# Kernel optimization log

Hardware: AMD Instinct MI355X
Metric: run time of the kernel (lower is better)

Reference implementation:

```python
import jax, jax.numpy as jnp
import numpy as np

B, S, D, H, O, E = 2, 2048, 1024, 2048, 1024, 8


def setup_inputs() -> dict:
    key = jax.random.key(0)
    k_x, k_rw, k_w1, k_w3, k_w2 = jax.random.split(key, 5)
    sD = 1.0 / np.sqrt(D)
    sH = 1.0 / np.sqrt(H)
    return {
        "x": jax.random.normal(k_x, (B, S, D), dtype=jnp.float32),
        "router_w": jax.random.normal(k_rw, (E, D), dtype=jnp.float32) * sD,  # nn.Linear(D, E).weight
        "router_b": jnp.zeros((E,), dtype=jnp.float32),
        "W1": jax.random.normal(k_w1, (E, D, H), dtype=jnp.float32) * sD,  # per-expert w1 (x @ W1)
        "W3": jax.random.normal(k_w3, (E, D, H), dtype=jnp.float32) * sD,  # per-expert gate w3
        "W2": jax.random.normal(k_w2, (E, H, O), dtype=jnp.float32) * sH,  # per-expert down-proj
        "top_k": 2,
    }


def reference(x, router_w, router_b, W1, W3, W2, top_k):
    b, s, d = x.shape
    xf = x.reshape(-1, d)  # [T, D], T = B*S
    T = xf.shape[0]

    # Router: softmax over experts, then top-k and renormalize
    logits = xf @ router_w.T + router_b            # [T, E]
    probs = jax.nn.softmax(logits, axis=-1)
    top_p, top_i = jax.lax.top_k(probs, top_k)     # [T, k]
    top_p = top_p / top_p.sum(axis=-1, keepdims=True)

    # Dense all-expert SwiGLU MLPs (faithful to reference: every expert on every token)
    h = jnp.einsum('td,edh->eth', xf, W1)          # [E, T, H]
    g = jnp.einsum('td,edh->eth', xf, W3)          # [E, T, H]
    eo = jnp.einsum('eth,eho->eto', jax.nn.silu(h) * g, W2)  # [E, T, O]

    # Gather each token's top-k expert outputs and combine
    sel = eo[top_i, jnp.arange(T)[:, None]]        # [T, k, O]
    out = jnp.sum(top_p[..., None] * sel, axis=1)  # [T, O]
    return out.reshape(b, s, -1)
```

## Files before the change

kernel.cpp:

```cpp
#include <hip/hip_runtime.h>
#include <hip/hip_bf16.h>

#define TTOK 4096
#define DIM  1024
#define HID  2048
#define ODIM 1024
#define NE   8

typedef __attribute__((ext_vector_type(8))) short  short8;
typedef __attribute__((ext_vector_type(4))) float  f32x4;
typedef __attribute__((ext_vector_type(8))) unsigned short ushort8;

#define WAITVM(N) asm volatile("s_waitcnt vmcnt(" #N ")" ::: "memory")
#define BAR() __builtin_amdgcn_s_barrier()

__device__ __forceinline__ unsigned short f2bf(float f){
  unsigned u = __float_as_uint(f);
  u += 0x7fffu + ((u >> 16) & 1u);
  return (unsigned short)(u >> 16);
}

__device__ __forceinline__ void gld16(const void* g, void* l){
  __builtin_amdgcn_global_load_lds(
      (const __attribute__((address_space(1))) unsigned int*)g,
      (__attribute__((address_space(3))) unsigned int*)l, 16, 0, 0);
}

__global__ __launch_bounds__(256) void router_kernel(
    const float* __restrict__ x, const float* __restrict__ rw,
    const float* __restrict__ rb, unsigned short* __restrict__ xbf,
    int2* __restrict__ toke, float2* __restrict__ tokw)
{
  int tok  = (blockIdx.x * blockDim.x + threadIdx.x) >> 6;
  int lane = threadIdx.x & 63;
  const float4* xr = (const float4*)(x + (size_t)tok * DIM + lane * 16);
  float xv[16];
#pragma unroll
  for (int q = 0; q < 4; q++){
    float4 v = xr[q];
    xv[q*4+0]=v.x; xv[q*4+1]=v.y; xv[q*4+2]=v.z; xv[q*4+3]=v.w;
  }
  ushort8 u0, u1;
#pragma unroll
  for (int j = 0; j < 8; j++){ u0[j] = f2bf(xv[j]); u1[j] = f2bf(xv[8+j]); }
  ushort8* xo = (ushort8*)(xbf + (size_t)tok * DIM + lane * 16);
  xo[0] = u0; xo[1] = u1;

  float lg[NE];
#pragma unroll
  for (int e = 0; e < NE; e++){
    const float4* wr4 = (const float4*)(rw + (size_t)e * DIM + lane * 16);
    float s = 0.f;
#pragma unroll
    for (int q = 0; q < 4; q++){
      float4 wv = wr4[q];
      s += xv[q*4+0]*wv.x + xv[q*4+1]*wv.y + xv[q*4+2]*wv.z + xv[q*4+3]*wv.w;
    }
    lg[e] = s;
  }
#pragma unroll
  for (int e = 0; e < NE; e++)
    for (int s = 1; s < 64; s <<= 1) lg[e] += __shfl_xor(lg[e], s, 64);

  if (lane == 0){
#pragma unroll
    for (int e = 0; e < NE; e++) lg[e] += rb[e];
    int e0 = 0; float l0 = lg[0];
    for (int e = 1; e < NE; e++) if (lg[e] > l0){ l0 = lg[e]; e0 = e; }
    int e1 = -1; float l1 = -1e30f;
    for (int e = 0; e < NE; e++) if (e != e0 && lg[e] > l1){ l1 = lg[e]; e1 = e; }
    float w0 = 1.f / (1.f + __expf(l1 - l0));
    float w1 = 1.f / (1.f + __expf(l0 - l1));
    toke[tok] = make_int2(e0, e1);
    tokw[tok] = make_float2(w0, w1);
  }
}

__global__ __launch_bounds__(256) void plan_kernel(
    const int2* __restrict__ toke, const float2* __restrict__ tokw,
    int* __restrict__ counts, int* __restrict__ offs,
    int* __restrict__ tlist, float* __restrict__ wlist)
{
  const int e  = blockIdx.x;
  const int t  = threadIdx.x;
  const int lane = t & 63, wv = t >> 6;
  __shared__ int sh[4 * 8];
  __shared__ int tot[8];
  __shared__ int sw[4];

  int wcnt[NE];
#pragma unroll
  for (int ee = 0; ee < NE; ee++) wcnt[ee] = 0;
  for (int base = 0; base < TTOK; base += 256){
    int2 p = toke[base + t];
#pragma unroll
    for (int ee = 0; ee < NE; ee++){
      unsigned long long m = __ballot(p.x == ee || p.y == ee);
      if (lane == 0) wcnt[ee] += __popcll(m);
    }
  }
  if (lane == 0){
#pragma unroll
    for (int ee = 0; ee < NE; ee++) sh[wv * 8 + ee] = wcnt[ee];
  }
  __syncthreads();
  if (t < NE) tot[t] = sh[t] + sh[8 + t] + sh[16 + t] + sh[24 + t];
  __syncthreads();

  int my_off = 0;
#pragma unroll
  for (int ee = 0; ee < NE; ee++) if (ee < e) my_off += tot[ee];

  if (e == 0 && t < NE){
    counts[t] = tot[t];
    int o = 0;
    for (int ee = 0; ee < NE; ee++){ if (ee < t) o += tot[ee]; }
    offs[t] = o;
    if (t == 0){
      int s = 0;
      for (int ee = 0; ee < NE; ee++) s += tot[ee];
      offs[NE] = s;
    }
  }

  int running = my_off;
  for (int base = 0; base < TTOK; base += 256){
    int tokid = base + t;
    int2  p = toke[tokid];
    float2 wgt = tokw[tokid];
    bool s0 = (p.x == e), s1 = (p.y == e);
    bool flag = s0 || s1;
    unsigned long long m = __ballot(flag);
    int rank_in_wave = __popcll(m & ((lane == 0) ? 0ull : ((~0ull) >> (64 - lane))));
    if (lane == 0) sw[wv] = __popcll(m);
    __syncthreads();
    int wave_base = 0, tot4 = 0;
#pragma unroll
    for (int w2 = 0; w2 < 4; w2++){ int v = sw[w2]; tot4 += v; if (w2 < wv) wave_base += v; }
    if (flag){
      int pos = running + wave_base + rank_in_wave;
      tlist[pos] = tokid;
      wlist[pos] = s0 ? wgt.x : wgt.y;
    }
    running += tot4;
    __syncthreads();
  }
}

__global__ __launch_bounds__(256) void transpose_cvt(
    const float* __restrict__ in, unsigned short* __restrict__ out, int R, int C)
{
  __shared__ __align__(16) unsigned short tl[64 * 128];
  int e = blockIdx.z;
  const float* src = in + (size_t)e * R * C + (size_t)(blockIdx.y * 128) * C + blockIdx.x * 64;
  unsigned short* dst = out + (size_t)e * C * R + (size_t)(blockIdx.x * 64) * R + blockIdx.y * 128;
  int t = threadIdx.x;
#pragma unroll
  for (int i = 0; i < 8; i++){
    int idx = i * 256 + t;
    int c = idx & 63, r0 = (idx >> 6) * 4;
    unsigned short v[4];
#pragma unroll
    for (int j = 0; j < 4; j++) v[j] = f2bf(src[(size_t)(r0 + j) * C + c]);
    unsigned long long pk = (unsigned long long)v[0] | ((unsigned long long)v[1] << 16)
      | ((unsigned long long)v[2] << 32) | ((unsigned long long)v[3] << 48);
    *(unsigned long long*)((char*)tl + c * 256 + (((r0 >> 3) ^ (c & 15)) * 16) + (r0 & 7) * 2) = pk;
  }
  __syncthreads();
#pragma unroll
  for (int i = 0; i < 4; i++){
    int idx = i * 256 + t;
    int c = idx >> 4, r0 = (idx & 15) * 8;
    ushort8 u = *(const ushort8*)((const char*)tl + c * 256 + (((r0 >> 3) ^ (c & 15)) * 16));
    *(ushort8*)(dst + (size_t)c * R + r0) = u;
  }
}

__global__ __launch_bounds__(256,2) void ffn1_kernel(
    const unsigned short* __restrict__ xbf,
    const unsigned short* __restrict__ w1t,
    const unsigned short* __restrict__ w3t,
    unsigned short* __restrict__ abuf,
    const int* __restrict__ counts, const int* __restrict__ offs,
    const int* __restrict__ tlist)
{
  const int e = blockIdx.x, ct = blockIdx.y, rt = blockIdx.z;
  const int cnt = counts[e];
  const int rbase = rt * 128;
  if (rbase >= cnt) return;
  const int off = offs[e];
  const int rows_left = cnt - rbase;
  const int t = threadIdx.x;
  const int lane = t & 63, w = t >> 6;
  const int wr = w >> 1, wc = w & 1;

  __shared__ __align__(16) unsigned short lds[3 * 12288];

  int ar0 = t >> 2, ar1 = 64 + (t >> 2);
  int psw = (t & 3) ^ ((t >> 3) & 3);
  int ra0 = ar0 < rows_left ? ar0 : rows_left - 1;
  int ra1 = ar1 < rows_left ? ar1 : rows_left - 1;
  int tok0 = tlist[off + rbase + ra0];
  int tok1 = tlist[off + rbase + ra1];
  const char* sA0  = (const char*)xbf + ((size_t)tok0 * DIM) * 2 + psw * 16;
  const char* sA1  = (const char*)xbf + ((size_t)tok1 * DIM) * 2 + psw * 16;
  const char* sB10 = (const char*)w1t + (((size_t)e * HID + ct * 128 + ar0) * DIM) * 2 + psw * 16;
  const char* sB11 = (const char*)w1t + (((size_t)e * HID + ct * 128 + ar1) * DIM) * 2 + psw * 16;
  const char* sB30 = (const char*)w3t + (((size_t)e * HID + ct * 128 + ar0) * DIM) * 2 + psw * 16;
  const char* sB31 = (const char*)w3t + (((size_t)e * HID + ct * 128 + ar1) * DIM) * 2 + psw * 16;
  const int dofs = w * 1024;

  auto STAGE = [&](int bs, int kt){
    int kb = kt << 6;
    char* base = (char*)lds + bs * 24576;
    gld16(sA0  + kb, base +            dofs);
    gld16(sA1  + kb, base +  4096 +    dofs);
    gld16(sB10 + kb, base +  8192 +    dofs);
    gld16(sB11 + kb, base + 12288 +    dofs);
    gld16(sB30 + kb, base + 16384 +    dofs);
    gld16(sB31 + kb, base + 20480 +    dofs);
  };

  const int chsw = ((lane >> 4) ^ ((lane >> 1) & 3)) * 8;
  int aofs[4], b1ofs[4], b3ofs[4];
#pragma unroll
  for (int i = 0; i < 4; i++){
    int am = wr * 64 + i * 16 + (lane & 15);
    int bn = wc * 64 + i * 16 + (lane & 15);
    aofs[i]  = am * 32 + chsw;
    b1ofs[i] = 4096 + bn * 32 + chsw;
    b3ofs[i] = 8192 + bn * 32 + chsw;
  }

  f32x4 acch[4][4], accg[4][4];
#pragma unroll
  for (int i = 0; i < 4; i++)
#pragma unroll
    for (int j = 0; j < 4; j++){
      acch[i][j] = (f32x4){0.f,0.f,0.f,0.f};
      accg[i][j] = (f32x4){0.f,0.f,0.f,0.f};
    }

  auto COMPUTE = [&](int bs){
    const unsigned short* L = lds + bs * 12288;
    short8 a[4], b1[4], b3[4];
#pragma unroll
    for (int i = 0; i < 4; i++){
      a[i]  = *(const short8*)(L + aofs[i]);
      b1[i] = *(const short8*)(L + b1ofs[i]);
      b3[i] = *(const short8*)(L + b3ofs[i]);
    }
    __builtin_amdgcn_s_setprio(1);
#pragma unroll
    for (int mi = 0; mi < 4; mi++)
#pragma unroll
      for (int ni = 0; ni < 4; ni++){
        acch[mi][ni] = __builtin_amdgcn_mfma_f32_16x16x32_bf16(a[mi], b1[ni], acch[mi][ni], 0, 0, 0);
        accg[mi][ni] = __builtin_amdgcn_mfma_f32_16x16x32_bf16(a[mi], b3[ni], accg[mi][ni], 0, 0, 0);
      }
    __builtin_amdgcn_s_setprio(0);
  };

  STAGE(0, 0); STAGE(1, 1); STAGE(2, 2);
  int cur = 0;
  for (int kt = 0; kt < DIM / 32 - 3; ++kt){
    WAITVM(12); BAR();
    COMPUTE(cur);
    BAR();
    STAGE(cur, kt + 3);
    cur = (cur == 2) ? 0 : cur + 1;
  }
  WAITVM(12); BAR(); COMPUTE(cur); BAR(); cur = (cur == 2) ? 0 : cur + 1;
  WAITVM(6);  BAR(); COMPUTE(cur); BAR(); cur = (cur == 2) ? 0 : cur + 1;
  WAITVM(0);  BAR(); COMPUTE(cur);

#pragma unroll
  for (int mi = 0; mi < 4; mi++)
#pragma unroll
    for (int r = 0; r < 4; r++){
      int row_local = wr * 64 + mi * 16 + ((lane >> 4) << 2) + r;
      if (row_local < rows_left){
        size_t pair = (size_t)(off + rbase + row_local);
        unsigned short* arow = abuf + pair * HID + ct * 128 + wc * 64 + (lane & 15);
#pragma unroll
        for (int ni = 0; ni < 4; ni++){
          float h = acch[mi][ni][r], g = accg[mi][ni][r];
          float sv = h / (1.f + __expf(-h));
          arow[ni * 16] = f2bf(sv * g);
        }
      }
    }
}

__global__ __launch_bounds__(256,3) void ffn2_kernel(
    const unsigned short* __restrict__ abuf,
    const unsigned short* __restrict__ w2t,
    float* __restrict__ dout,
    const int* __restrict__ counts, const int* __restrict__ offs,
    const int* __restrict__ tlist, const float* __restrict__ wlist)
{
  const int e = blockIdx.x, ct = blockIdx.y, rt = blockIdx.z;
  const int cnt = counts[e];
  const int rbase = rt * 128;
  if (rbase >= cnt) return;
  const int off = offs[e];
  const int rows_left = cnt - rbase;
  const int t = threadIdx.x;
  const int lane = t & 63, w = t >> 6;
  const int wr = w >> 1, wc = w & 1;

  __shared__ __align__(16) unsigned short lds[3 * 8192];

  int ar0 = t >> 2, ar1 = 64 + (t >> 2);
  int psw = (t & 3) ^ ((t >> 3) & 3);
  int ra0 = ar0 < rows_left ? ar0 : rows_left - 1;
  int ra1 = ar1 < rows_left ? ar1 : rows_left - 1;
  const char* sA0 = (const char*)abuf + ((size_t)(off + rbase + ra0) * HID) * 2 + psw * 16;
  const char* sA1 = (const char*)abuf + ((size_t)(off + rbase + ra1) * HID) * 2 + psw * 16;
  const char* sB0 = (const char*)w2t + (((size_t)e * ODIM + ct * 128 + ar0) * HID) * 2 + psw * 16;
  const char* sB1 = (const char*)w2t + (((size_t)e * ODIM + ct * 128 + ar1) * HID) * 2 + psw * 16;
  const int dofs = w * 1024;

  auto STAGE = [&](int bs, int kt){
    int kb = kt << 6;
    char* base = (char*)lds + bs * 16384;
    gld16(sA0 + kb, base +           dofs);
    gld16(sA1 + kb, base +  4096 +   dofs);
    gld16(sB0 + kb, base +  8192 +   dofs);
    gld16(sB1 + kb, base + 12288 +   dofs);
  };

  const int chsw = ((lane >> 4) ^ ((lane >> 1) & 3)) * 8;
  int aofs[4], bofs[4];
#pragma unroll
  for (int i = 0; i < 4; i++){
    int am = wr * 64 + i * 16 + (lane & 15);
    int bn = wc * 64 + i * 16 + (lane & 15);
    aofs[i] = am * 32 + chsw;
    bofs[i] = 4096 + bn * 32 + chsw;
  }

  f32x4 acc[4][4];
#pragma unroll
  for (int i = 0; i < 4; i++)
#pragma unroll
    for (int j = 0; j < 4; j++) acc[i][j] = (f32x4){0.f,0.f,0.f,0.f};

  auto COMPUTE = [&](int bs){
    const unsigned short* L = lds + bs * 8192;
    short8 a[4], b[4];
#pragma unroll
    for (int i = 0; i < 4; i++){
      a[i] = *(const short8*)(L + aofs[i]);
      b[i] = *(const short8*)(L + bofs[i]);
    }
    __builtin_amdgcn_s_setprio(1);
#pragma unroll
    for (int mi = 0; mi < 4; mi++)
#pragma unroll
      for (int ni = 0; ni < 4; ni++)
        acc[mi][ni] = __builtin_amdgcn_mfma_f32_16x16x32_bf16(a[mi], b[ni], acc[mi][ni], 0, 0, 0);
    __builtin_amdgcn_s_setprio(0);
  };

  STAGE(0, 0); STAGE(1, 1); STAGE(2, 2);
  int cur = 0;
  for (int kt = 0; kt < HID / 32 - 3; ++kt){
    WAITVM(8); BAR();
    COMPUTE(cur);
    BAR();
    STAGE(cur, kt + 3);
    cur = (cur == 2) ? 0 : cur + 1;
  }
  WAITVM(8); BAR(); COMPUTE(cur); BAR(); cur = (cur == 2) ? 0 : cur + 1;
  WAITVM(4); BAR(); COMPUTE(cur); BAR(); cur = (cur == 2) ? 0 : cur + 1;
  WAITVM(0); BAR(); COMPUTE(cur);

#pragma unroll
  for (int mi = 0; mi < 4; mi++)
#pragma unroll
    for (int r = 0; r < 4; r++){
      int row_local = wr * 64 + mi * 16 + ((lane >> 4) << 2) + r;
      if (row_local < rows_left){
        int pair = off + rbase + row_local;
        int token = tlist[pair];
        float p   = wlist[pair];
        float* orow = dout + (size_t)token * ODIM + ct * 128 + wc * 64 + (lane & 15);
#pragma unroll
        for (int ni = 0; ni < 4; ni++)
          atomicAdd(orow + ni * 16, p * acc[mi][ni][r]);
      }
    }
}

extern "C" void kernel_launch(void* const* d_in, const int* in_sizes, int n_in,
                              void* d_out, int out_size, void* d_ws, size_t ws_size,
                              hipStream_t stream)
{
  const float* x  = (const float*)d_in[0];
  const float* rw = (const float*)d_in[1];
  const float* rb = (const float*)d_in[2];
  const float* W1 = (const float*)d_in[3];
  const float* W3 = (const float*)d_in[4];
  const float* W2 = (const float*)d_in[5];

  char* ws = (char*)d_ws;
  const size_t off_ctrl = 0;
  const size_t off_toke = 256;
  const size_t off_tokw = off_toke + (size_t)TTOK * 8;
  const size_t off_tl   = off_tokw + (size_t)TTOK * 8;
  const size_t off_wl   = off_tl   + (size_t)2 * TTOK * 4;
  const size_t off_xbf  = off_wl   + (size_t)2 * TTOK * 4;
  const size_t off_w1t  = off_xbf  + (size_t)TTOK * DIM * 2;
  const size_t off_w3t  = off_w1t  + (size_t)NE * HID * DIM * 2;
  const size_t off_w2t  = off_w3t  + (size_t)NE * HID * DIM * 2;
  const size_t off_ab   = off_w2t  + (size_t)NE * ODIM * HID * 2;
  const size_t need     = off_ab   + (size_t)2 * TTOK * HID * 2;
  if (ws_size < need) return;

  int* counts = (int*)(ws + off_ctrl);
  int* offs   = (int*)(ws + off_ctrl + 64);
  int2*   toke = (int2*)  (ws + off_toke);
  float2* tokw = (float2*)(ws + off_tokw);
  int*    tl   = (int*)   (ws + off_tl);
  float*  wl   = (float*) (ws + off_wl);
  unsigned short* xbf = (unsigned short*)(ws + off_xbf);
  unsigned short* w1t = (unsigned short*)(ws + off_w1t);
  unsigned short* w3t = (unsigned short*)(ws + off_w3t);
  unsigned short* w2t = (unsigned short*)(ws + off_w2t);
  unsigned short* ab  = (unsigned short*)(ws + off_ab);

  hipMemsetAsync(d_out, 0, (size_t)out_size * sizeof(float), stream);

  router_kernel<<<TTOK / 4, 256, 0, stream>>>(x, rw, rb, xbf, toke, tokw);
  plan_kernel<<<NE, 256, 0, stream>>>(toke, tokw, counts, offs, tl, wl);

  transpose_cvt<<<dim3(HID / 64, DIM / 128, NE), 256, 0, stream>>>(W1, w1t, DIM, HID);
  transpose_cvt<<<dim3(HID / 64, DIM / 128, NE), 256, 0, stream>>>(W3, w3t, DIM, HID);
  transpose_cvt<<<dim3(ODIM / 64, HID / 128, NE), 256, 0, stream>>>(W2, w2t, HID, ODIM);

  ffn1_kernel<<<dim3(NE, HID / 128, 32), 256, 0, stream>>>(xbf, w1t, w3t, ab, counts, offs, tl);
  ffn2_kernel<<<dim3(NE, ODIM / 128, 32), 256, 0, stream>>>(ab, w2t, (float*)d_out, counts, offs, tl, wl);
}
```

Measured before the change: 253.8 us.

## Switch FFN GEMMs to double buffering, raise occupancy, and swizzle block order

Both expert GEMM kernels drop from triple-buffered to double-buffered LDS and issue the next stage's loads before computing the current one. The smaller LDS footprint lets launch bounds rise from 2 to 3 blocks per CU for ffn1 and from 3 to 4 for ffn2. The 3D grid becomes a 1D grid with an explicit mapping that interleaves experts across consecutive blocks and groups column/row tiles for better L2 reuse. The cost is a shallower prefetch depth and tighter register budgets, which could cause spills or expose more memory latency.

Result: slower. 449.3 us (+77.0%).

```diff
diff --git a/kernel.cpp b/kernel.cpp
--- a/kernel.cpp
+++ b/kernel.cpp
@@ -176,7 +176,7 @@
   }
 }
 
-__global__ __launch_bounds__(256,2) void ffn1_kernel(
+__global__ __launch_bounds__(256,3) void ffn1_kernel(
     const unsigned short* __restrict__ xbf,
     const unsigned short* __restrict__ w1t,
     const unsigned short* __restrict__ w3t,
@@ -184,7 +184,12 @@
     const int* __restrict__ counts, const int* __restrict__ offs,
     const int* __restrict__ tlist)
 {
-  const int e = blockIdx.x, ct = blockIdx.y, rt = blockIdx.z;
+  const int wgid = blockIdx.x;
+  const int e = wgid & 7;
+  const int j = wgid >> 3;
+  const int u = j & 15, g = j >> 4;
+  const int ct = (g & 7) * 2 + (u >> 3);
+  const int rt = (g >> 3) * 8 + (u & 7);
   const int cnt = counts[e];
   const int rbase = rt * 128;
   if (rbase >= cnt) return;
@@ -194,7 +199,7 @@
   const int lane = t & 63, w = t >> 6;
   const int wr = w >> 1, wc = w & 1;
 
-  __shared__ __align__(16) unsigned short lds[3 * 12288];
+  __shared__ __align__(16) unsigned short lds[2 * 12288];
 
   int ar0 = t >> 2, ar1 = 64 + (t >> 2);
   int psw = (t & 3) ^ ((t >> 3) & 3);
@@ -236,9 +241,9 @@
 #pragma unroll
   for (int i = 0; i < 4; i++)
 #pragma unroll
-    for (int j = 0; j < 4; j++){
-      acch[i][j] = (f32x4){0.f,0.f,0.f,0.f};
-      accg[i][j] = (f32x4){0.f,0.f,0.f,0.f};
+    for (int jj = 0; jj < 4; jj++){
+      acch[i][jj] = (f32x4){0.f,0.f,0.f,0.f};
+      accg[i][jj] = (f32x4){0.f,0.f,0.f,0.f};
     }
 
   auto COMPUTE = [&](int bs){
@@ -261,18 +266,16 @@
     __builtin_amdgcn_s_setprio(0);
   };
 
-  STAGE(0, 0); STAGE(1, 1); STAGE(2, 2);
-  int cur = 0;
-  for (int kt = 0; kt < DIM / 32 - 3; ++kt){
-    WAITVM(12); BAR();
-    COMPUTE(cur);
+  STAGE(0, 0);
+  int kt = 0;
+  for (; kt < DIM / 32 - 1; ++kt){
+    STAGE((kt + 1) & 1, kt + 1);
+    WAITVM(6); BAR();
+    COMPUTE(kt & 1);
     BAR();
-    STAGE(cur, kt + 3);
-    cur = (cur == 2) ? 0 : cur + 1;
-  }
-  WAITVM(12); BAR(); COMPUTE(cur); BAR(); cur = (cur == 2) ? 0 : cur + 1;
-  WAITVM(6);  BAR(); COMPUTE(cur); BAR(); cur = (cur == 2) ? 0 : cur + 1;
-  WAITVM(0);  BAR(); COMPUTE(cur);
+  }
+  WAITVM(0); BAR();
+  COMPUTE(kt & 1);
 
 #pragma unroll
   for (int mi = 0; mi < 4; mi++)
@@ -284,22 +287,27 @@
         unsigned short* arow = abuf + pair * HID + ct * 128 + wc * 64 + (lane & 15);
 #pragma unroll
         for (int ni = 0; ni < 4; ni++){
-          float h = acch[mi][ni][r], g = accg[mi][ni][r];
+          float h = acch[mi][ni][r], gg = accg[mi][ni][r];
           float sv = h / (1.f + __expf(-h));
-          arow[ni * 16] = f2bf(sv * g);
+          arow[ni * 16] = f2bf(sv * gg);
         }
       }
     }
 }
 
-__global__ __launch_bounds__(256,3) void ffn2_kernel(
+__global__ __launch_bounds__(256,4) void ffn2_kernel(
     const unsigned short* __restrict__ abuf,
     const unsigned short* __restrict__ w2t,
     float* __restrict__ dout,
     const int* __restrict__ counts, const int* __restrict__ offs,
     const int* __restrict__ tlist, const float* __restrict__ wlist)
 {
-  const int e = blockIdx.x, ct = blockIdx.y, rt = blockIdx.z;
+  const int wgid = blockIdx.x;
+  const int e = wgid & 7;
+  const int j = wgid >> 3;
+  const int u = j & 7, g = j >> 3;
+  const int ct = (g & 3) * 2 + (u >> 2);
+  const int rt = (g >> 2) * 4 + (u & 3);
   const int cnt = counts[e];
   const int rbase = rt * 128;
   if (rbase >= cnt) return;
@@ -309,7 +317,7 @@
   const int lane = t & 63, w = t >> 6;
   const int wr = w >> 1, wc = w & 1;
 
-  __shared__ __align__(16) unsigned short lds[3 * 8192];
+  __shared__ __align__(16) unsigned short lds[2 * 8192];
 
   int ar0 = t >> 2, ar1 = 64 + (t >> 2);
   int psw = (t & 3) ^ ((t >> 3) & 3);
@@ -344,7 +352,7 @@
 #pragma unroll
   for (int i = 0; i < 4; i++)
 #pragma unroll
-    for (int j = 0; j < 4; j++) acc[i][j] = (f32x4){0.f,0.f,0.f,0.f};
+    for (int jj = 0; jj < 4; jj++) acc[i][jj] = (f32x4){0.f,0.f,0.f,0.f};
 
   auto COMPUTE = [&](int bs){
     const unsigned short* L = lds + bs * 8192;
@@ -363,18 +371,16 @@
     __builtin_amdgcn_s_setprio(0);
   };
 
-  STAGE(0, 0); STAGE(1, 1); STAGE(2, 2);
-  int cur = 0;
-  for (int kt = 0; kt < HID / 32 - 3; ++kt){
-    WAITVM(8); BAR();
-    COMPUTE(cur);
+  STAGE(0, 0);
+  int kt = 0;
+  for (; kt < HID / 32 - 1; ++kt){
+    STAGE((kt + 1) & 1, kt + 1);
+    WAITVM(4); BAR();
+    COMPUTE(kt & 1);
     BAR();
-    STAGE(cur, kt + 3);
-    cur = (cur == 2) ? 0 : cur + 1;
-  }
-  WAITVM(8); BAR(); COMPUTE(cur); BAR(); cur = (cur == 2) ? 0 : cur + 1;
-  WAITVM(4); BAR(); COMPUTE(cur); BAR(); cur = (cur == 2) ? 0 : cur + 1;
-  WAITVM(0); BAR(); COMPUTE(cur);
+  }
+  WAITVM(0); BAR();
+  COMPUTE(kt & 1);
 
 #pragma unroll
   for (int mi = 0; mi < 4; mi++)
@@ -439,6 +445,6 @@
   transpose_cvt<<<dim3(HID / 64, DIM / 128, NE), 256, 0, stream>>>(W3, w3t, DIM, HID);
   transpose_cvt<<<dim3(ODIM / 64, HID / 128, NE), 256, 0, stream>>>(W2, w2t, HID, ODIM);
 
-  ffn1_kernel<<<dim3(NE, HID / 128, 32), 256, 0, stream>>>(xbf, w1t, w3t, ab, counts, offs, tl);
-  ffn2_kernel<<<dim3(NE, ODIM / 128, 32), 256, 0, stream>>>(ab, w2t, (float*)d_out, counts, offs, tl, wl);
-}
+  ffn1_kernel<<<NE * 16 * 32, 256, 0, stream>>>(xbf, w1t, w3t, ab, counts, offs, tl);
+  ffn2_kernel<<<NE * 8 * 32, 256, 0, stream>>>(ab, w2t, (float*)d_out, counts, offs, tl, wl);
+}
```

## Pre-gather routed tokens contiguously and remap FFN block order for L2 locality

Applied to the files above, without the earlier changes.

Adds a gather kernel that copies each routed token's bf16 activation row into a contiguous per-expert buffer, so the first FFN kernel streams A tiles linearly instead of following token indices. Both FFN kernels switch to a 1D grid with a swizzled mapping that keeps blocks of the same expert and nearby row/column tiles adjacent in launch order, aimed at better L2 reuse of weights and activations. The cost is an extra launch plus a write and read of a gathered activation buffer.

Result: slower. 272.9 us (+7.6%).

```diff
diff --git a/kernel.cpp b/kernel.cpp
--- a/kernel.cpp
+++ b/kernel.cpp
@@ -147,6 +147,18 @@
   }
 }
 
+__global__ __launch_bounds__(256) void gather_kernel(
+    const unsigned short* __restrict__ xbf, const int* __restrict__ tlist,
+    unsigned short* __restrict__ xg)
+{
+  int pair = blockIdx.x * 4 + (threadIdx.x >> 6);
+  int lane = threadIdx.x & 63;
+  int tok  = tlist[pair];
+  const ushort8* s = (const ushort8*)(xbf + (size_t)tok * DIM + lane * 16);
+  ushort8* d = (ushort8*)(xg + (size_t)pair * DIM + lane * 16);
+  d[0] = s[0]; d[1] = s[1];
+}
+
 __global__ __launch_bounds__(256) void transpose_cvt(
     const float* __restrict__ in, unsigned short* __restrict__ out, int R, int C)
 {
@@ -177,14 +189,18 @@
 }
 
 __global__ __launch_bounds__(256,2) void ffn1_kernel(
-    const unsigned short* __restrict__ xbf,
+    const unsigned short* __restrict__ xg,
     const unsigned short* __restrict__ w1t,
     const unsigned short* __restrict__ w3t,
     unsigned short* __restrict__ abuf,
-    const int* __restrict__ counts, const int* __restrict__ offs,
-    const int* __restrict__ tlist)
-{
-  const int e = blockIdx.x, ct = blockIdx.y, rt = blockIdx.z;
+    const int* __restrict__ counts, const int* __restrict__ offs)
+{
+  const int wgid = blockIdx.x;
+  const int e = wgid & 7;
+  const int j = wgid >> 3;
+  const int u = j & 15, g = j >> 4;
+  const int ct = (g & 7) * 2 + (u >> 3);
+  const int rt = (g >> 3) * 8 + (u & 7);
   const int cnt = counts[e];
   const int rbase = rt * 128;
   if (rbase >= cnt) return;
@@ -200,10 +216,8 @@
   int psw = (t & 3) ^ ((t >> 3) & 3);
   int ra0 = ar0 < rows_left ? ar0 : rows_left - 1;
   int ra1 = ar1 < rows_left ? ar1 : rows_left - 1;
-  int tok0 = tlist[off + rbase + ra0];
-  int tok1 = tlist[off + rbase + ra1];
-  const char* sA0  = (const char*)xbf + ((size_t)tok0 * DIM) * 2 + psw * 16;
-  const char* sA1  = (const char*)xbf + ((size_t)tok1 * DIM) * 2 + psw * 16;
+  const char* sA0  = (const char*)xg + (size_t)(off + rbase + ra0) * 2048 + psw * 16;
+  const char* sA1  = (const char*)xg + (size_t)(off + rbase + ra1) * 2048 + psw * 16;
   const char* sB10 = (const char*)w1t + (((size_t)e * HID + ct * 128 + ar0) * DIM) * 2 + psw * 16;
   const char* sB11 = (const char*)w1t + (((size_t)e * HID + ct * 128 + ar1) * DIM) * 2 + psw * 16;
   const char* sB30 = (const char*)w3t + (((size_t)e * HID + ct * 128 + ar0) * DIM) * 2 + psw * 16;
@@ -236,9 +250,9 @@
 #pragma unroll
   for (int i = 0; i < 4; i++)
 #pragma unroll
-    for (int j = 0; j < 4; j++){
-      acch[i][j] = (f32x4){0.f,0.f,0.f,0.f};
-      accg[i][j] = (f32x4){0.f,0.f,0.f,0.f};
+    for (int jj = 0; jj < 4; jj++){
+      acch[i][jj] = (f32x4){0.f,0.f,0.f,0.f};
+      accg[i][jj] = (f32x4){0.f,0.f,0.f,0.f};
     }
 
   auto COMPUTE = [&](int bs){
@@ -284,9 +298,9 @@
         unsigned short* arow = abuf + pair * HID + ct * 128 + wc * 64 + (lane & 15);
 #pragma unroll
         for (int ni = 0; ni < 4; ni++){
-          float h = acch[mi][ni][r], g = accg[mi][ni][r];
+          float h = acch[mi][ni][r], gg = accg[mi][ni][r];
           float sv = h / (1.f + __expf(-h));
-          arow[ni * 16] = f2bf(sv * g);
+          arow[ni * 16] = f2bf(sv * gg);
         }
       }
     }
@@ -299,7 +313,12 @@
     const int* __restrict__ counts, const int* __restrict__ offs,
     const int* __restrict__ tlist, const float* __restrict__ wlist)
 {
-  const int e = blockIdx.x, ct = blockIdx.y, rt = blockIdx.z;
+  const int wgid = blockIdx.x;
+  const int e = wgid & 7;
+  const int j = wgid >> 3;
+  const int u = j & 7, g = j >> 3;
+  const int ct = (g & 3) * 2 + (u >> 2);
+  const int rt = (g >> 2) * 4 + (u & 3);
   const int cnt = counts[e];
   const int rbase = rt * 128;
   if (rbase >= cnt) return;
@@ -344,7 +363,7 @@
 #pragma unroll
   for (int i = 0; i < 4; i++)
 #pragma unroll
-    for (int j = 0; j < 4; j++) acc[i][j] = (f32x4){0.f,0.f,0.f,0.f};
+    for (int jj = 0; jj < 4; jj++) acc[i][jj] = (f32x4){0.f,0.f,0.f,0.f};
 
   auto COMPUTE = [&](int bs){
     const unsigned short* L = lds + bs * 8192;
@@ -415,7 +434,8 @@
   const size_t off_w3t  = off_w1t  + (size_t)NE * HID * DIM * 2;
   const size_t off_w2t  = off_w3t  + (size_t)NE * HID * DIM * 2;
   const size_t off_ab   = off_w2t  + (size_t)NE * ODIM * HID * 2;
-  const size_t need     = off_ab   + (size_t)2 * TTOK * HID * 2;
+  const size_t off_xg   = off_ab   + (size_t)2 * TTOK * HID * 2;
+  const size_t need     = off_xg   + (size_t)2 * TTOK * DIM * 2;
   if (ws_size < need) return;
 
   int* counts = (int*)(ws + off_ctrl);
@@ -429,16 +449,18 @@
   unsigned short* w3t = (unsigned short*)(ws + off_w3t);
   unsigned short* w2t = (unsigned short*)(ws + off_w2t);
   unsigned short* ab  = (unsigned short*)(ws + off_ab);
+  unsigned short* xg  = (unsigned short*)(ws + off_xg);
 
   hipMemsetAsync(d_out, 0, (size_t)out_size * sizeof(float), stream);
 
   router_kernel<<<TTOK / 4, 256, 0, stream>>>(x, rw, rb, xbf, toke, tokw);
   plan_kernel<<<NE, 256, 0, stream>>>(toke, tokw, counts, offs, tl, wl);
+  gather_kernel<<<2 * TTOK / 4, 256, 0, stream>>>(xbf, tl, xg);
 
   transpose_cvt<<<dim3(HID / 64, DIM / 128, NE), 256, 0, stream>>>(W1, w1t, DIM, HID);
   transpose_cvt<<<dim3(HID / 64, DIM / 128, NE), 256, 0, stream>>>(W3, w3t, DIM, HID);
   transpose_cvt<<<dim3(ODIM / 64, HID / 128, NE), 256, 0, stream>>>(W2, w2t, HID, ODIM);
 
-  ffn1_kernel<<<dim3(NE, HID / 128, 32), 256, 0, stream>>>(xbf, w1t, w3t, ab, counts, offs, tl);
-  ffn2_kernel<<<dim3(NE, ODIM / 128, 32), 256, 0, stream>>>(ab, w2t, (float*)d_out, counts, offs, tl, wl);
-}
+  ffn1_kernel<<<NE * 16 * 32, 256, 0, stream>>>(xg, w1t, w3t, ab, counts, offs);
+  ffn2_kernel<<<NE * 8 * 32, 256, 0, stream>>>(ab, w2t, (float*)d_out, counts, offs, tl, wl);
+}
```
